# Optimization experiments

Hardware: AMD Instinct MI355X
Metric: run time of the kernel (lower is better)

The kernel has to match this reference:

```python
import jax, jax.numpy as jnp
import numpy as np

D_MODEL = 1024
D_INNER = 2048   # expand_factor * d_model
D_STATE = 16
D_CONV = 4
DT_RANK = 64     # ceil(d_model / 16)
EPS = 1e-5


def setup_inputs() -> dict:
    key = jax.random.key(0)
    ks = jax.random.split(key, 10)
    B, L = 2, 1024
    w = lambda k, shape, s: (jax.random.normal(k, shape, jnp.float32) * s)
    A = jnp.tile(jnp.arange(1, D_STATE + 1, dtype=jnp.float32), (D_INNER, 1))
    return {
        "hidden_states": jax.random.normal(ks[0], (B, L, D_MODEL), jnp.float32),
        "norm_w": jnp.ones((D_MODEL,), jnp.float32),
        "norm_b": jnp.zeros((D_MODEL,), jnp.float32),
        "in_proj_w": w(ks[1], (D_MODEL, 2 * D_INNER), 0.02),
        "conv_w": w(ks[2], (D_INNER, D_CONV), 0.2),
        "conv_b": jnp.zeros((D_INNER,), jnp.float32),
        "x_proj_w": w(ks[3], (D_INNER, DT_RANK + 2 * D_STATE), 0.02),
        "dt_proj_w": w(ks[4], (DT_RANK, D_INNER), 0.1),
        "dt_proj_b": w(ks[5], (D_INNER,), 0.1),
        "A_log": jnp.log(A),
        "D_param": jnp.ones((D_INNER,), jnp.float32),
        "out_proj_w": w(ks[6], (D_INNER, D_MODEL), 0.02),
    }


def _causal_depthwise_conv(x, conv_w, conv_b):
    # x: [B, L, d_inner] -> causal depthwise conv, kernel size D_CONV
    B, L, C = x.shape
    xt = jnp.transpose(x, (0, 2, 1))                 # [B, C, L]
    xt = jnp.pad(xt, ((0, 0), (0, 0), (D_CONV - 1, 0)))  # left pad == torch pad+truncate
    k = conv_w[:, None, :]                            # [C, 1, K] (OIH, groups=C)
    y = jax.lax.conv_general_dilated(
        xt, k, window_strides=(1,), padding="VALID",
        dimension_numbers=("NCH", "OIH", "NCH"), feature_group_count=C)
    y = y + conv_b[None, :, None]
    return jnp.transpose(y, (0, 2, 1))                # [B, L, C]


def _selective_scan(u, delta, A, Bm, Cm, D_param):
    # u, delta: [B, L, d_inner]; A: [d_inner, d_state]; Bm, Cm: [B, L, d_state]
    dA = jnp.exp(delta[..., None] * A[None, None])            # [B,L,d,n]
    dBu = delta[..., None] * Bm[:, :, None, :] * u[..., None]  # [B,L,d,n]
    h0 = jnp.zeros((u.shape[0], u.shape[2], A.shape[1]), u.dtype)

    def step(h, inp):
        dA_t, dBu_t, c_t = inp          # [B,d,n], [B,d,n], [B,n]
        h = dA_t * h + dBu_t
        y = jnp.einsum("bdn,bn->bd", h, c_t)
        return h, y

    xs = (jnp.moveaxis(dA, 1, 0), jnp.moveaxis(dBu, 1, 0), jnp.moveaxis(Cm, 1, 0))
    _, ys = jax.lax.scan(step, h0, xs)   # ys: [L, B, d]
    y = jnp.moveaxis(ys, 0, 1)           # [B, L, d]
    return y + u * D_param[None, None]


def reference(hidden_states, norm_w, norm_b, in_proj_w, conv_w, conv_b,
              x_proj_w, dt_proj_w, dt_proj_b, A_log, D_param, out_proj_w):
    h = hidden_states
    mu = jnp.mean(h, axis=-1, keepdims=True)
    var = jnp.mean(jnp.square(h - mu), axis=-1, keepdims=True)
    h = (h - mu) * jax.lax.rsqrt(var + EPS) * norm_w + norm_b

    xz = h @ in_proj_w                       # [B,L,2*d_inner]
    x, z = jnp.split(xz, 2, axis=-1)
    x = _causal_depthwise_conv(x, conv_w, conv_b)
    x = jax.nn.silu(x)

    A = -jnp.exp(A_log)                      # [d_inner, d_state]
    xp = x @ x_proj_w                        # [B,L,dt_rank+2*d_state]
    dt_r = xp[..., :DT_RANK]
    Bm = xp[..., DT_RANK:DT_RANK + D_STATE]
    Cm = xp[..., DT_RANK + D_STATE:]
    delta = jax.nn.softplus(dt_r @ dt_proj_w + dt_proj_b)  # [B,L,d_inner]

    y = _selective_scan(x, delta, A, Bm, Cm, D_param)
    y = y * jax.nn.silu(z)
    return y @ out_proj_w
```

## Files before the change

kernel.cpp:

```cpp
#include <hip/hip_runtime.h>
#include <hip/hip_bf16.h>

#define D_MODEL 1024
#define D_INNER 2048
#define D_STATE 16
#define DT_RANK 64
#define NB 2
#define LSEQ 1024
#define NROWS (NB * LSEQ)
#define XPN 96
#define NC 32
#define CL 32

typedef __attribute__((ext_vector_type(8))) short bf16x8;
typedef __attribute__((ext_vector_type(4))) float f32x4;

__device__ __forceinline__ unsigned short f2bf(float x) {
    __hip_bfloat16 h = __float2bfloat16(x);
    return *reinterpret_cast<unsigned short*>(&h);
}
__device__ __forceinline__ float bf2f(unsigned short u) {
    unsigned int v = ((unsigned int)u) << 16;
    float f;
    __builtin_memcpy(&f, &v, 4);
    return f;
}
__device__ __forceinline__ unsigned short f2h(float x) {
    _Float16 h = (_Float16)x;
    unsigned short u;
    __builtin_memcpy(&u, &h, 2);
    return u;
}
__device__ __forceinline__ float h2f(unsigned short u) {
    _Float16 h;
    __builtin_memcpy(&h, &u, 2);
    return (float)h;
}

__global__ __launch_bounds__(256) void wcast_ln(const float* __restrict__ W0, unsigned short* __restrict__ D0,
                                                const float* __restrict__ W1, unsigned short* __restrict__ D1,
                                                const float* __restrict__ W2, unsigned short* __restrict__ D2,
                                                const float* __restrict__ W3, unsigned short* __restrict__ D3,
                                                const float* __restrict__ hx, const float* __restrict__ nw,
                                                const float* __restrict__ nb, unsigned short* __restrict__ lnout) {
    int bid = blockIdx.x;
    if (bid >= 6528) {
        int row = bid - 6528;
        const float4* xr = (const float4*)(hx + (size_t)row * D_MODEL);
        float4 v = xr[threadIdx.x];
        float s = v.x + v.y + v.z + v.w;
        float sq = v.x * v.x + v.y * v.y + v.z * v.z + v.w * v.w;
#pragma unroll
        for (int off = 32; off > 0; off >>= 1) {
            s += __shfl_down(s, off);
            sq += __shfl_down(sq, off);
        }
        __shared__ float ws[4], wq[4];
        __shared__ float smu, srstd;
        int wave = threadIdx.x >> 6;
        if ((threadIdx.x & 63) == 0) { ws[wave] = s; wq[wave] = sq; }
        __syncthreads();
        if (threadIdx.x == 0) {
            float ts = ws[0] + ws[1] + ws[2] + ws[3];
            float tq = wq[0] + wq[1] + wq[2] + wq[3];
            float mu = ts * (1.f / D_MODEL);
            float var = tq * (1.f / D_MODEL) - mu * mu;
            smu = mu;
            srstd = rsqrtf(var + 1e-5f);
        }
        __syncthreads();
        float mu = smu, rstd = srstd;
        float4 wv = ((const float4*)nw)[threadIdx.x];
        float4 bv = ((const float4*)nb)[threadIdx.x];
        ushort4 pk;
        pk.x = f2bf((v.x - mu) * rstd * wv.x + bv.x);
        pk.y = f2bf((v.y - mu) * rstd * wv.y + bv.y);
        pk.z = f2bf((v.z - mu) * rstd * wv.z + bv.z);
        pk.w = f2bf((v.w - mu) * rstd * wv.w + bv.w);
        *(ushort4*)(lnout + (size_t)row * D_MODEL + threadIdx.x * 4) = pk;
        return;
    }
    const float* W;
    unsigned short* Dst;
    int K, Nreal, bx, by;
    if (bid < 4096) { W = W0; Dst = D0; K = 1024; Nreal = 4096; bx = bid & 127; by = bid >> 7; }
    else if (bid < 4352) { int j = bid - 4096; W = W1; Dst = D1; K = 2048; Nreal = 96; bx = j & 3; by = j >> 2; }
    else if (bid < 6400) { int j = bid - 4352; W = W2; Dst = D2; K = 2048; Nreal = 1024; bx = j & 31; by = j >> 5; }
    else { int j = bid - 6400; W = W3; Dst = D3; K = 64; Nreal = 2048; bx = j & 63; by = j >> 6; }
    __shared__ float t[32][33];
    int tn = bx * 32, tk = by * 32;
    for (int e = threadIdx.x; e < 1024; e += 256) {
        int r = e >> 5, c = e & 31;
        int n = tn + c;
        t[r][c] = (n < Nreal) ? W[(size_t)(tk + r) * Nreal + n] : 0.f;
    }
    __syncthreads();
    for (int e = threadIdx.x; e < 1024; e += 256) {
        int r = e >> 5, c = e & 31;
        Dst[(size_t)(tn + r) * K + tk + c] = f2bf(t[c][r]);
    }
}

template <int EPI>
__global__ __launch_bounds__(256) void gemm_bf16(const unsigned short* __restrict__ A,
                                                 const unsigned short* __restrict__ Bt,
                                                 const float* __restrict__ bias,
                                                 float* __restrict__ C,
                                                 void* __restrict__ C2,
                                                 int M, int K, int ldc, int Nreal) {
    __shared__ unsigned short As[128 * 64];
    __shared__ unsigned short Bs[128 * 64];
    int nwg = gridDim.x * gridDim.y;
    int orig = blockIdx.y * gridDim.x + blockIdx.x;
    int q = nwg >> 3, r = nwg & 7;
    int xcd = orig & 7, idx = orig >> 3;
    int newid = (xcd < r ? xcd * (q + 1) : r * (q + 1) + (xcd - r) * q) + idx;
    int bx = newid % gridDim.x, by = newid / gridDim.x;

    int tid = threadIdx.x;
    int lane = tid & 63;
    int wave = tid >> 6;
    int wr = (wave >> 1) * 64, wc = (wave & 1) * 64;
    int bm = by * 128, bn = bx * 128;
    int kchunk = K / gridDim.z;
    int kbeg = blockIdx.z * kchunk;

    f32x4 acc[4][4];
#pragma unroll
    for (int i = 0; i < 4; ++i)
#pragma unroll
        for (int j = 0; j < 4; ++j) acc[i][j] = (f32x4){0.f, 0.f, 0.f, 0.f};

    int ar = lane & 15;
    int kq = lane >> 4;

    for (int k0 = kbeg; k0 < kbeg + kchunk; k0 += 64) {
        __syncthreads();
#pragma unroll
        for (int s = 0; s < 4; ++s) {
            int seg = s * 256 + tid;
            int row = seg >> 3, p = seg & 7;
            int c = p ^ (row & 7);
            __builtin_amdgcn_global_load_lds(
                (const __attribute__((address_space(1))) void*)(A + (size_t)(bm + row) * K + k0 + c * 8),
                (__attribute__((address_space(3))) void*)(As + seg * 8), 16, 0, 0);
        }
#pragma unroll
        for (int s = 0; s < 4; ++s) {
            int seg = s * 256 + tid;
            int row = seg >> 3, p = seg & 7;
            int c = p ^ (row & 7);
            __builtin_amdgcn_global_load_lds(
                (const __attribute__((address_space(1))) void*)(Bt + (size_t)(bn + row) * K + k0 + c * 8),
                (__attribute__((address_space(3))) void*)(Bs + seg * 8), 16, 0, 0);
        }
        __syncthreads();
#pragma unroll
        for (int kk = 0; kk < 2; ++kk) {
            bf16x8 af[4], bfr[4];
#pragma unroll
            for (int i = 0; i < 4; ++i) {
                int row = wr + i * 16 + ar;
                int pos = ((kk << 2) | kq) ^ (row & 7);
                af[i] = *(const bf16x8*)&As[(size_t)row * 64 + pos * 8];
            }
#pragma unroll
            for (int j = 0; j < 4; ++j) {
                int row = wc + j * 16 + ar;
                int pos = ((kk << 2) | kq) ^ (row & 7);
                bfr[j] = *(const bf16x8*)&Bs[(size_t)row * 64 + pos * 8];
            }
#pragma unroll
            for (int i = 0; i < 4; ++i)
#pragma unroll
                for (int j = 0; j < 4; ++j)
                    acc[i][j] = __builtin_amdgcn_mfma_f32_16x16x32_bf16(af[i], bfr[j], acc[i][j], 0, 0, 0);
        }
    }

    int crow0 = bm + wr + (lane >> 4) * 4;
    int ccol0 = bn + wc + (lane & 15);
    size_t zoff = (size_t)blockIdx.z * (size_t)M * ldc;
#pragma unroll
    for (int i = 0; i < 4; ++i)
#pragma unroll
        for (int j = 0; j < 4; ++j) {
            int col = ccol0 + j * 16;
            if (EPI == 0) {
                if (col < Nreal) {
                    float* cp = C + zoff + (size_t)(crow0 + i * 16) * ldc + col;
#pragma unroll
                    for (int rr = 0; rr < 4; ++rr) cp[(size_t)rr * ldc] = acc[i][j][rr];
                }
            } else if (EPI == 2) {
                unsigned short* cx = (unsigned short*)C;
                unsigned short* cz = (unsigned short*)C2;
                if (col < 2048) {
#pragma unroll
                    for (int rr = 0; rr < 4; ++rr)
                        cx[(size_t)(crow0 + i * 16 + rr) * 2048 + col] = f2bf(acc[i][j][rr]);
                } else {
#pragma unroll
                    for (int rr = 0; rr < 4; ++rr)
                        cz[(size_t)(crow0 + i * 16 + rr) * 2048 + (col - 2048)] = f2bf(acc[i][j][rr]);
                }
            } else if (EPI == 3) {
                if (col < Nreal) {
                    unsigned short* cp = (unsigned short*)C2 + zoff + (size_t)(crow0 + i * 16) * ldc + col;
#pragma unroll
                    for (int rr = 0; rr < 4; ++rr) cp[(size_t)rr * ldc] = f2h(acc[i][j][rr]);
                }
            } else {
                float bv = bias[col];
                unsigned short* cp = (unsigned short*)C2 + (size_t)(crow0 + i * 16) * ldc + col;
#pragma unroll
                for (int rr = 0; rr < 4; ++rr) {
                    float v = acc[i][j][rr] + bv;
                    v = (v > 20.f) ? v : log1pf(__expf(v));
                    cp[(size_t)rr * ldc] = f2bf(v);
                }
            }
        }
}

__global__ __launch_bounds__(256) void reduce_xp(const unsigned short* __restrict__ part,
                                                 float* __restrict__ xp,
                                                 unsigned short* __restrict__ dtr) {
    int t = blockIdx.x * 256 + threadIdx.x;
    float s = 0.f;
#pragma unroll
    for (int k = 0; k < 16; ++k) s += h2f(part[(size_t)k * ((size_t)NROWS * XPN) + t]);
    xp[t] = s;
    int row = t / 96, col = t - row * 96;
    if (col < 64) dtr[(size_t)row * 64 + col] = f2bf(s);
}

__global__ __launch_bounds__(256) void reduce_out(const unsigned short* __restrict__ part,
                                                  float* __restrict__ out) {
    int t = blockIdx.x * 256 + threadIdx.x;
    const size_t stride = (size_t)NROWS * D_MODEL;
    ushort4 p0 = ((const ushort4*)part)[t];
    ushort4 p1 = ((const ushort4*)(part + stride))[t];
    ushort4 p2 = ((const ushort4*)(part + 2 * stride))[t];
    ushort4 p3 = ((const ushort4*)(part + 3 * stride))[t];
    float4 o;
    o.x = h2f(p0.x) + h2f(p1.x) + h2f(p2.x) + h2f(p3.x);
    o.y = h2f(p0.y) + h2f(p1.y) + h2f(p2.y) + h2f(p3.y);
    o.z = h2f(p0.z) + h2f(p1.z) + h2f(p2.z) + h2f(p3.z);
    o.w = h2f(p0.w) + h2f(p1.w) + h2f(p2.w) + h2f(p3.w);
    ((float4*)out)[t] = o;
}

__global__ __launch_bounds__(256) void conv_silu_kernel(const unsigned short* __restrict__ xx,
                                                        const float* __restrict__ cw,
                                                        const float* __restrict__ cb,
                                                        unsigned short* __restrict__ outb) {
    int gid = blockIdx.x * 256 + threadIdx.x;
    int d4 = (gid & 511) << 2;
    int bl = gid >> 9;
    int l = bl & (LSEQ - 1);
    const unsigned short* base = xx + (size_t)bl * D_INNER + d4;
    ushort4 zr4 = {0, 0, 0, 0};
    ushort4 X0 = *(const ushort4*)base;
    ushort4 X1 = (l >= 1) ? *(const ushort4*)(base - D_INNER) : zr4;
    ushort4 X2 = (l >= 2) ? *(const ushort4*)(base - 2 * D_INNER) : zr4;
    ushort4 X3 = (l >= 3) ? *(const ushort4*)(base - 3 * D_INNER) : zr4;
    float4 bias = *(const float4*)(cb + d4);
    const float4* wv = (const float4*)(cw + (size_t)d4 * 4);
    float xs0[4] = {bf2f(X0.x), bf2f(X0.y), bf2f(X0.z), bf2f(X0.w)};
    float xs1[4] = {bf2f(X1.x), bf2f(X1.y), bf2f(X1.z), bf2f(X1.w)};
    float xs2[4] = {bf2f(X2.x), bf2f(X2.y), bf2f(X2.z), bf2f(X2.w)};
    float xs3[4] = {bf2f(X3.x), bf2f(X3.y), bf2f(X3.z), bf2f(X3.w)};
    float bs[4] = {bias.x, bias.y, bias.z, bias.w};
    ushort4 ob;
    unsigned short* obp = (unsigned short*)&ob;
#pragma unroll
    for (int e = 0; e < 4; ++e) {
        float4 we = wv[e];
        float acc = bs[e];
        acc = fmaf(we.w, xs0[e], acc);
        acc = fmaf(we.z, xs1[e], acc);
        acc = fmaf(we.y, xs2[e], acc);
        acc = fmaf(we.x, xs3[e], acc);
        obp[e] = f2bf(acc / (1.f + __expf(-acc)));
    }
    *(ushort4*)(outb + (size_t)bl * D_INNER + d4) = ob;
}

__global__ __launch_bounds__(256) void scan_local(const float* __restrict__ xp,
                                                  const unsigned short* __restrict__ delta,
                                                  const unsigned short* __restrict__ ub,
                                                  const float* __restrict__ A_log,
                                                  float* __restrict__ hst,
                                                  float* __restrict__ sdel) {
    int bc = blockIdx.x >> 3;
    int b = bc >> 5, c = bc & (NC - 1);
    int d = (blockIdx.x & 7) * 256 + threadIdx.x;
    int base_r = b * LSEQ + c * CL;
    __shared__ float Bsm[CL * 16];
    for (int e = threadIdx.x; e < CL * 4; e += 256) {
        int l = e >> 2, q4 = e & 3;
        float4 v = *(const float4*)&xp[(size_t)(base_r + l) * XPN + DT_RANK + q4 * 4];
        *(float4*)&Bsm[l * 16 + q4 * 4] = v;
    }
    __syncthreads();
    float Av[16];
    const float4* ap = (const float4*)(A_log + (size_t)d * 16);
#pragma unroll
    for (int qq = 0; qq < 4; ++qq) {
        float4 a = ap[qq];
        Av[4 * qq + 0] = -__expf(a.x); Av[4 * qq + 1] = -__expf(a.y);
        Av[4 * qq + 2] = -__expf(a.z); Av[4 * qq + 3] = -__expf(a.w);
    }
    float h[16] = {};
    float sd = 0.f;
    const unsigned short* dp = delta + (size_t)base_r * D_INNER + d;
    const unsigned short* up = ub + (size_t)base_r * D_INNER + d;
#pragma unroll 4
    for (int l = 0; l < CL; ++l) {
        float dv = bf2f(dp[(size_t)l * D_INNER]);
        float u = bf2f(up[(size_t)l * D_INNER]);
        float du = dv * u;
        sd += dv;
#pragma unroll
        for (int n = 0; n < 16; ++n) {
            float dA = __expf(dv * Av[n]);
            h[n] = fmaf(dA, h[n], du * Bsm[l * 16 + n]);
        }
    }
    size_t hi = ((size_t)(c * NB + b) * D_INNER + d) * 16;
#pragma unroll
    for (int qq = 0; qq < 4; ++qq) {
        float4 v = make_float4(h[4 * qq], h[4 * qq + 1], h[4 * qq + 2], h[4 * qq + 3]);
        *(float4*)(hst + hi + 4 * qq) = v;
    }
    sdel[(size_t)(c * NB + b) * D_INNER + d] = sd;
}

__global__ __launch_bounds__(256) void scan_combine(const float* __restrict__ A_log,
                                                    const float* __restrict__ sdel,
                                                    float* __restrict__ hst) {
    __shared__ float hl[NC][256];
    __shared__ float sl[NC][16];
    int b = blockIdx.x >> 7;
    int d0 = (blockIdx.x & 127) * 16;
    int t = threadIdx.x;
    int dd = t >> 4;
    for (int e = t; e < NC * 256; e += 256) {
        int c = e >> 8, tt = e & 255;
        hl[c][tt] = hst[(size_t)(c * NB + b) * (D_INNER * 16) + d0 * 16 + tt];
    }
    for (int e = t; e < NC * 16; e += 256) {
        int c = e >> 4, ddd = e & 15;
        sl[c][ddd] = sdel[(size_t)(c * NB + b) * D_INNER + d0 + ddd];
    }
    __syncthreads();
    float Avn = -__expf(A_log[(size_t)d0 * 16 + t]);
    float h = 0.f;
#pragma unroll
    for (int c = 0; c < NC; ++c) {
        float S = sl[c][dd];
        float tmp = hl[c][t];
        hl[c][t] = h;
        h = fmaf(__expf(Avn * S), h, tmp);
    }
    __syncthreads();
    for (int e = t; e < NC * 256; e += 256) {
        int c = e >> 8, tt = e & 255;
        hst[(size_t)(c * NB + b) * (D_INNER * 16) + d0 * 16 + tt] = hl[c][tt];
    }
}

__global__ __launch_bounds__(256) void scan_final(const float* __restrict__ xp,
                                                  const unsigned short* __restrict__ delta,
                                                  const unsigned short* __restrict__ ub,
                                                  const unsigned short* __restrict__ zb,
                                                  const float* __restrict__ hst,
                                                  const float* __restrict__ A_log,
                                                  const float* __restrict__ Dp,
                                                  unsigned short* __restrict__ yb) {
    int bc = blockIdx.x >> 3;
    int b = bc >> 5, c = bc & (NC - 1);
    int d = (blockIdx.x & 7) * 256 + threadIdx.x;
    int base_r = b * LSEQ + c * CL;
    __shared__ float Bsm[CL * 16], Csm[CL * 16];
    for (int e = threadIdx.x; e < CL * 8; e += 256) {
        int l = e >> 3, q8 = e & 7;
        float4 v = *(const float4*)&xp[(size_t)(base_r + l) * XPN + DT_RANK + q8 * 4];
        if (q8 < 4) *(float4*)&Bsm[l * 16 + q8 * 4] = v;
        else *(float4*)&Csm[l * 16 + (q8 - 4) * 4] = v;
    }
    __syncthreads();
    float Av[16];
    const float4* ap = (const float4*)(A_log + (size_t)d * 16);
#pragma unroll
    for (int qq = 0; qq < 4; ++qq) {
        float4 a = ap[qq];
        Av[4 * qq + 0] = -__expf(a.x); Av[4 * qq + 1] = -__expf(a.y);
        Av[4 * qq + 2] = -__expf(a.z); Av[4 * qq + 3] = -__expf(a.w);
    }
    float h[16];
    size_t hi = ((size_t)(c * NB + b) * D_INNER + d) * 16;
#pragma unroll
    for (int qq = 0; qq < 4; ++qq) {
        float4 v = *(const float4*)(hst + hi + 4 * qq);
        h[4 * qq] = v.x; h[4 * qq + 1] = v.y; h[4 * qq + 2] = v.z; h[4 * qq + 3] = v.w;
    }
    float Dv = Dp[d];
    const unsigned short* dp = delta + (size_t)base_r * D_INNER + d;
    const unsigned short* up = ub + (size_t)base_r * D_INNER + d;
    const unsigned short* zp = zb + (size_t)base_r * D_INNER + d;
#pragma unroll 4
    for (int l = 0; l < CL; ++l) {
        float dv = bf2f(dp[(size_t)l * D_INNER]);
        float u = bf2f(up[(size_t)l * D_INNER]);
        float du = dv * u;
        float acc = 0.f;
#pragma unroll
        for (int n = 0; n < 16; ++n) {
            float dA = __expf(dv * Av[n]);
            h[n] = fmaf(dA, h[n], du * Bsm[l * 16 + n]);
            acc = fmaf(h[n], Csm[l * 16 + n], acc);
        }
        float yv = fmaf(u, Dv, acc);
        float zv = bf2f(zp[(size_t)l * D_INNER]);
        float sz = zv / (1.f + __expf(-zv));
        yb[(size_t)(base_r + l) * D_INNER + d] = f2bf(yv * sz);
    }
}

extern "C" void kernel_launch(void* const* d_in, const int* in_sizes, int n_in,
                              void* d_out, int out_size, void* d_ws, size_t ws_size,
                              hipStream_t stream) {
    const float* hidden = (const float*)d_in[0];
    const float* norm_w = (const float*)d_in[1];
    const float* norm_b = (const float*)d_in[2];
    const float* in_proj_w = (const float*)d_in[3];
    const float* conv_w = (const float*)d_in[4];
    const float* conv_b = (const float*)d_in[5];
    const float* x_proj_w = (const float*)d_in[6];
    const float* dt_proj_w = (const float*)d_in[7];
    const float* dt_proj_b = (const float*)d_in[8];
    const float* A_log = (const float*)d_in[9];
    const float* D_param = (const float*)d_in[10];
    const float* out_proj_w = (const float*)d_in[11];
    float* out = (float*)d_out;

    float* wsf = (float*)d_ws;
    unsigned short* hbufb = (unsigned short*)wsf;
    float* xpbuf = wsf;
    float* sdelbuf = wsf + 196608;
    unsigned short* xb = (unsigned short*)(wsf + 1048576);
    float* hst = wsf + 1048576;
    unsigned short* zb = (unsigned short*)(wsf + 3145728);
    unsigned short* ub = (unsigned short*)(wsf + 5242880);
    unsigned short* yb = ub;
    unsigned short* wAt = (unsigned short*)(wsf + 7340032);
    unsigned short* xpart16 = (unsigned short*)(wsf + 7340032);
    unsigned short* opart = (unsigned short*)(wsf + 7340032);
    unsigned short* wXt = (unsigned short*)(wsf + 10485760);
    unsigned short* wDt = (unsigned short*)(wsf + 10616832);
    unsigned short* dtrb = (unsigned short*)(wsf + 10682368);
    unsigned short* deltab = (unsigned short*)(wsf + 11665408);
    unsigned short* wOt = (unsigned short*)(wsf + 13762560);

    wcast_ln<<<6528 + NROWS, 256, 0, stream>>>(in_proj_w, wAt, x_proj_w, wXt, out_proj_w, wOt,
                                               dt_proj_w, wDt, hidden, norm_w, norm_b, hbufb);

    gemm_bf16<2><<<dim3(4096 / 128, NROWS / 128, 1), 256, 0, stream>>>(
        hbufb, wAt, nullptr, (float*)xb, zb, NROWS, 1024, 2048, 4096);

    conv_silu_kernel<<<(NROWS * D_INNER) / 1024, 256, 0, stream>>>(xb, conv_w, conv_b, ub);

    gemm_bf16<3><<<dim3(1, NROWS / 128, 16), 256, 0, stream>>>(
        ub, wXt, nullptr, nullptr, xpart16, NROWS, 2048, XPN, XPN);

    reduce_xp<<<(NROWS * XPN) / 256, 256, 0, stream>>>(xpart16, xpbuf, dtrb);

    gemm_bf16<4><<<dim3(D_INNER / 128, NROWS / 128, 1), 256, 0, stream>>>(
        dtrb, wDt, dt_proj_b, nullptr, deltab, NROWS, 64, D_INNER, D_INNER);

    scan_local<<<NB * NC * (D_INNER / 256), 256, 0, stream>>>(
        xpbuf, deltab, ub, A_log, hst, sdelbuf);
    scan_combine<<<256, 256, 0, stream>>>(A_log, sdelbuf, hst);
    scan_final<<<NB * NC * (D_INNER / 256), 256, 0, stream>>>(
        xpbuf, deltab, ub, zb, hst, A_log, D_param, yb);

    gemm_bf16<3><<<dim3(1024 / 128, NROWS / 128, 4), 256, 0, stream>>>(
        yb, wOt, nullptr, nullptr, opart, NROWS, 2048, 1024, 1024);

    reduce_out<<<(NROWS * D_MODEL / 4) / 256, 256, 0, stream>>>(opart, out);
}
```

Baseline: 166.9 us.

## Drop XCD block remap, widen conv loads to 8 elements, trim xp stores

Removes the XCD-aware workgroup remapping in the bf16 GEMM so blocks use their native grid indices. The conv+SiLU kernel now handles 8 channels per thread with 16-byte vector loads and stores, halving the grid. reduce_xp writes the fp32 xp buffer only for the B/C columns, since the dt columns go to the bf16 buffer. Dropping the remap may reduce L2 locality across XCDs, and any consumer that read dt columns from xp would now see stale data.

After: 166.6 us (median of 2 runs). Within noise of the previous version (-0.2%).

```diff
diff --git a/kernel.cpp b/kernel.cpp
--- a/kernel.cpp
+++ b/kernel.cpp
@@ -13,6 +13,7 @@
 #define CL 32
 
 typedef __attribute__((ext_vector_type(8))) short bf16x8;
+typedef __attribute__((ext_vector_type(8))) unsigned short u16x8;
 typedef __attribute__((ext_vector_type(4))) float f32x4;
 
 __device__ __forceinline__ unsigned short f2bf(float x) {
@@ -110,12 +111,7 @@
                                                  int M, int K, int ldc, int Nreal) {
     __shared__ unsigned short As[128 * 64];
     __shared__ unsigned short Bs[128 * 64];
-    int nwg = gridDim.x * gridDim.y;
-    int orig = blockIdx.y * gridDim.x + blockIdx.x;
-    int q = nwg >> 3, r = nwg & 7;
-    int xcd = orig & 7, idx = orig >> 3;
-    int newid = (xcd < r ? xcd * (q + 1) : r * (q + 1) + (xcd - r) * q) + idx;
-    int bx = newid % gridDim.x, by = newid / gridDim.x;
+    int bx = blockIdx.x, by = blockIdx.y;
 
     int tid = threadIdx.x;
     int lane = tid & 63;
@@ -230,9 +226,9 @@
     float s = 0.f;
 #pragma unroll
     for (int k = 0; k < 16; ++k) s += h2f(part[(size_t)k * ((size_t)NROWS * XPN) + t]);
-    xp[t] = s;
     int row = t / 96, col = t - row * 96;
     if (col < 64) dtr[(size_t)row * 64 + col] = f2bf(s);
+    else xp[t] = s;
 }
 
 __global__ __launch_bounds__(256) void reduce_out(const unsigned short* __restrict__ part,
@@ -256,35 +252,27 @@
                                                         const float* __restrict__ cb,
                                                         unsigned short* __restrict__ outb) {
     int gid = blockIdx.x * 256 + threadIdx.x;
-    int d4 = (gid & 511) << 2;
-    int bl = gid >> 9;
+    int d8 = (gid & 255) << 3;
+    int bl = gid >> 8;
     int l = bl & (LSEQ - 1);
-    const unsigned short* base = xx + (size_t)bl * D_INNER + d4;
-    ushort4 zr4 = {0, 0, 0, 0};
-    ushort4 X0 = *(const ushort4*)base;
-    ushort4 X1 = (l >= 1) ? *(const ushort4*)(base - D_INNER) : zr4;
-    ushort4 X2 = (l >= 2) ? *(const ushort4*)(base - 2 * D_INNER) : zr4;
-    ushort4 X3 = (l >= 3) ? *(const ushort4*)(base - 3 * D_INNER) : zr4;
-    float4 bias = *(const float4*)(cb + d4);
-    const float4* wv = (const float4*)(cw + (size_t)d4 * 4);
-    float xs0[4] = {bf2f(X0.x), bf2f(X0.y), bf2f(X0.z), bf2f(X0.w)};
-    float xs1[4] = {bf2f(X1.x), bf2f(X1.y), bf2f(X1.z), bf2f(X1.w)};
-    float xs2[4] = {bf2f(X2.x), bf2f(X2.y), bf2f(X2.z), bf2f(X2.w)};
-    float xs3[4] = {bf2f(X3.x), bf2f(X3.y), bf2f(X3.z), bf2f(X3.w)};
-    float bs[4] = {bias.x, bias.y, bias.z, bias.w};
-    ushort4 ob;
-    unsigned short* obp = (unsigned short*)&ob;
-#pragma unroll
-    for (int e = 0; e < 4; ++e) {
-        float4 we = wv[e];
-        float acc = bs[e];
-        acc = fmaf(we.w, xs0[e], acc);
-        acc = fmaf(we.z, xs1[e], acc);
-        acc = fmaf(we.y, xs2[e], acc);
-        acc = fmaf(we.x, xs3[e], acc);
-        obp[e] = f2bf(acc / (1.f + __expf(-acc)));
-    }
-    *(ushort4*)(outb + (size_t)bl * D_INNER + d4) = ob;
+    const unsigned short* base = xx + (size_t)bl * D_INNER + d8;
+    u16x8 zr = {0, 0, 0, 0, 0, 0, 0, 0};
+    u16x8 X0 = *(const u16x8*)base;
+    u16x8 X1 = (l >= 1) ? *(const u16x8*)(base - D_INNER) : zr;
+    u16x8 X2 = (l >= 2) ? *(const u16x8*)(base - 2 * D_INNER) : zr;
+    u16x8 X3 = (l >= 3) ? *(const u16x8*)(base - 3 * D_INNER) : zr;
+    u16x8 ob;
+#pragma unroll
+    for (int e = 0; e < 8; ++e) {
+        float4 we = *(const float4*)(cw + (size_t)(d8 + e) * 4);
+        float acc = cb[d8 + e];
+        acc = fmaf(we.w, bf2f(X0[e]), acc);
+        acc = fmaf(we.z, bf2f(X1[e]), acc);
+        acc = fmaf(we.y, bf2f(X2[e]), acc);
+        acc = fmaf(we.x, bf2f(X3[e]), acc);
+        ob[e] = f2bf(acc / (1.f + __expf(-acc)));
+    }
+    *(u16x8*)(outb + (size_t)bl * D_INNER + d8) = ob;
 }
 
 __global__ __launch_bounds__(256) void scan_local(const float* __restrict__ xp,
@@ -470,7 +458,7 @@
     gemm_bf16<2><<<dim3(4096 / 128, NROWS / 128, 1), 256, 0, stream>>>(
         hbufb, wAt, nullptr, (float*)xb, zb, NROWS, 1024, 2048, 4096);
 
-    conv_silu_kernel<<<(NROWS * D_INNER) / 1024, 256, 0, stream>>>(xb, conv_w, conv_b, ub);
+    conv_silu_kernel<<<(NROWS * D_INNER) / 2048, 256, 0, stream>>>(xb, conv_w, conv_b, ub);
 
     gemm_bf16<3><<<dim3(1, NROWS / 128, 16), 256, 0, stream>>>(
         ub, wXt, nullptr, nullptr, xpart16, NROWS, 2048, XPN, XPN);
```
